# Kernel tuning notes

Hardware: AMD Instinct MI355X
Metric: run time of the kernel (lower is better)

## Reference

```python
import jax, jax.numpy as jnp
import numpy as np

N_HEAD = 16
D_MODEL = 1024
D_K = 64
D_V = 64
B = 8
L = 1024
EPS = 1e-5
NEG_INF = -1e9


def setup_inputs() -> dict:
    key = jax.random.key(0)
    ks = jax.random.split(key, 6)
    qkv_out = N_HEAD * (2 * D_K + D_V)  # 3072
    x = jax.random.normal(ks[0], (B, L, D_MODEL), dtype=jnp.float32)
    # causal attention mask (N, 1, L, L), 1 = keep, 0 = masked
    mask = jnp.broadcast_to(jnp.tril(jnp.ones((L, L), jnp.float32))[None, None], (B, 1, L, L))
    W_qkv = jax.random.normal(ks[1], (D_MODEL, qkv_out), dtype=jnp.float32) * 0.02
    b_qkv = jnp.zeros((qkv_out,), jnp.float32)
    W_proj = jax.random.normal(ks[2], (N_HEAD * D_V, D_MODEL), dtype=jnp.float32) * 0.02
    b_proj = jnp.zeros((D_MODEL,), jnp.float32)
    gamma = jnp.ones((D_MODEL,), jnp.float32)
    beta = jnp.zeros((D_MODEL,), jnp.float32)
    return {"x": x, "mask": mask, "W_qkv": W_qkv, "b_qkv": b_qkv,
            "W_proj": W_proj, "b_proj": b_proj, "gamma": gamma, "beta": beta}


def _layer_norm(x, gamma, beta):
    u = jnp.mean(x, axis=-1, keepdims=True)
    s = jnp.mean(jnp.square(x - u), axis=-1, keepdims=True)
    return gamma * (x - u) / jnp.sqrt(s + EPS) + beta


def reference(x, mask, W_qkv, b_qkv, W_proj, b_proj, gamma, beta):
    residual = x
    qkv = jnp.einsum('bld,df->blf', x, W_qkv) + b_qkv  # 1x1 Conv1D == pointwise linear
    q_l = N_HEAD * D_K
    q = qkv[:, :, :q_l]
    k = qkv[:, :, q_l:2 * q_l]
    v = qkv[:, :, 2 * q_l:]
    # split heads: (B, L, H*D) -> (B, H, L, D)
    q = q.reshape(B, L, N_HEAD, D_K).transpose(0, 2, 1, 3)
    k = k.reshape(B, L, N_HEAD, D_K).transpose(0, 2, 1, 3)
    v = v.reshape(B, L, N_HEAD, D_V).transpose(0, 2, 1, 3)
    temperature = np.power(D_K, 0.5)
    attn = jnp.einsum('bhqd,bhkd->bhqk', q, k) / temperature
    attn = mask * attn + (1.0 - mask) * NEG_INF
    attn = jax.nn.softmax(attn, axis=-1)  # dropout is identity in eval mode
    out = jnp.einsum('bhqk,bhkd->bhqd', attn, v)
    # merge heads: (B, H, L, Dv) -> (B, L, H*Dv)
    out = out.transpose(0, 2, 1, 3).reshape(B, L, N_HEAD * D_V)
    out = jnp.einsum('blf,fd->bld', out, W_proj) + b_proj
    out = _layer_norm(out + residual, gamma, beta)
    return out, attn
```

## Files before the change

### kernel.cpp

```cpp
#include <hip/hip_runtime.h>

typedef __attribute__((ext_vector_type(4))) float f32x4;
typedef __attribute__((ext_vector_type(8))) __bf16 bf16x8;
typedef __attribute__((ext_vector_type(8))) unsigned short ushort8;

static __device__ __forceinline__ unsigned short f2bf(float f) {
    unsigned int u = __float_as_uint(f);
    u += 0x7fffu + ((u >> 16) & 1u);
    return (unsigned short)(u >> 16);
}
static __device__ __forceinline__ float bf2f(unsigned short u) {
    return __uint_as_float((unsigned int)u << 16);
}
static __device__ __forceinline__ bf16x8 as_bf(ushort8 v) {
    union { ushort8 u; bf16x8 b; } x; x.u = v; return x.b;
}
static __device__ __forceinline__ void gll16(const void* g, void* l) {
    __builtin_amdgcn_global_load_lds(
        (const __attribute__((address_space(1))) void*)g,
        (__attribute__((address_space(3))) void*)l, 16, 0, 0);
}

__global__ void cvt_bf16(const float* __restrict__ in, unsigned short* __restrict__ out,
                         int n8) {
    int i = blockIdx.x * 256 + threadIdx.x;
    if (i >= n8) return;
    const float4* p = (const float4*)(in + (size_t)i * 8);
    float4 a = p[0], b = p[1];
    ushort8 o = { f2bf(a.x), f2bf(a.y), f2bf(a.z), f2bf(a.w),
                  f2bf(b.x), f2bf(b.y), f2bf(b.z), f2bf(b.w) };
    *(ushort8*)(out + (size_t)i * 8) = o;
}

__global__ void tconv_bf16(const float* __restrict__ in, unsigned short* __restrict__ out,
                           int K, int N) {
    __shared__ float t[64][65];
    const int tid = threadIdx.x;
    const int n0 = blockIdx.x * 64, k0 = blockIdx.y * 64;
#pragma unroll
    for (int i = 0; i < 4; i++) {
        int idx = tid + 256 * i;
        int r = idx >> 4, c4 = (idx & 15) * 4;
        float4 v = *(const float4*)(in + (size_t)(k0 + r) * N + n0 + c4);
        t[r][c4] = v.x; t[r][c4 + 1] = v.y; t[r][c4 + 2] = v.z; t[r][c4 + 3] = v.w;
    }
    __syncthreads();
#pragma unroll
    for (int i = 0; i < 2; i++) {
        int idx = tid + 256 * i;
        int nl = idx >> 3, k8 = (idx & 7) * 8;
        ushort8 o;
#pragma unroll
        for (int j = 0; j < 8; j++) o[j] = f2bf(t[k8 + j][nl]);
        *(ushort8*)(out + (size_t)(n0 + nl) * K + k0 + k8) = o;
    }
}

template <int EPI>
__global__ __launch_bounds__(256, 2)
void gemm_bf16(const unsigned short* __restrict__ A,
               const unsigned short* __restrict__ BT,
               const float* __restrict__ bias,
               unsigned short* __restrict__ qh, unsigned short* __restrict__ kh,
               unsigned short* __restrict__ vt,
               float* __restrict__ Cf,
               int K, int mtiles, int Ncols)
{
    __shared__ unsigned short smem[2 * 128 * 64];
    unsigned short* As = smem;
    unsigned short* Bs = smem + 128 * 64;

    const int tid = threadIdx.x;
    const int wid = tid >> 6, lane = tid & 63;
    const int g = lane >> 4, c = lane & 15;
    const int wr = (wid >> 1) * 64, wc = (wid & 1) * 64;

    const int nwg = gridDim.x;
    const int swz = ((int)blockIdx.x & 7) * (nwg >> 3) + ((int)blockIdx.x >> 3);
    const int bm = (swz % mtiles) * 128;
    const int bn = (swz / mtiles) * 128;

    const int srow = lane >> 3;
    const int scol8 = ((lane & 7) ^ srow) * 8;
    const size_t arow0 = (size_t)(bm + wid * 8 + srow);
    const size_t brow0 = (size_t)(bn + wid * 8 + srow);

    f32x4 acc[4][4] = {};

    for (int k0 = 0; k0 < K; k0 += 64) {
        __syncthreads();
#pragma unroll
        for (int t = 0; t < 4; t++) {
            gll16(A + (arow0 + t * 32) * K + k0 + scol8,
                  (char*)As + t * 4096 + wid * 1024);
            gll16(BT + (brow0 + t * 32) * K + k0 + scol8,
                  (char*)Bs + t * 4096 + wid * 1024);
        }
        __syncthreads();
#pragma unroll
        for (int ks = 0; ks < 2; ks++) {
            bf16x8 af[4], bfr[4];
#pragma unroll
            for (int mi = 0; mi < 4; mi++) {
                int row = wr + mi * 16 + c;
                int off = row * 128 + ((ks * 64 + g * 16) ^ ((c & 7) << 4));
                af[mi] = as_bf(*(const ushort8*)((const char*)As + off));
            }
#pragma unroll
            for (int ni = 0; ni < 4; ni++) {
                int row = wc + ni * 16 + c;
                int off = row * 128 + ((ks * 64 + g * 16) ^ ((c & 7) << 4));
                bfr[ni] = as_bf(*(const ushort8*)((const char*)Bs + off));
            }
#pragma unroll
            for (int mi = 0; mi < 4; mi++)
#pragma unroll
                for (int ni = 0; ni < 4; ni++)
                    acc[mi][ni] = __builtin_amdgcn_mfma_f32_16x16x32_bf16(
                        af[mi], bfr[ni], acc[mi][ni], 0, 0, 0);
        }
    }

    if (EPI == 1) {
#pragma unroll
        for (int mi = 0; mi < 4; mi++)
#pragma unroll
            for (int ni = 0; ni < 4; ni++)
#pragma unroll
                for (int r = 0; r < 4; r++) {
                    int m = bm + wr + mi * 16 + g * 4 + r;
                    int n = bn + wc + ni * 16 + c;
                    Cf[(size_t)m * Ncols + n] = acc[mi][ni][r] + bias[n];
                }
    } else {
        const int b = bm >> 10, lb = bm & 1023;
#pragma unroll
        for (int nh = 0; nh < 2; nh++) {
            int n0 = bn + nh * 64;
            int region = n0 >> 10;
            int h = (n0 & 1023) >> 6;
            __syncthreads();
            if (region < 2) {
                float qscale = (region == 0) ? 0.1803368801f : 1.0f;
                if ((wid & 1) == nh) {
#pragma unroll
                    for (int mi = 0; mi < 4; mi++)
#pragma unroll
                        for (int ni = 0; ni < 4; ni++)
#pragma unroll
                            for (int r = 0; r < 4; r++) {
                                int row = wr + mi * 16 + g * 4 + r;
                                int col = ni * 16 + c;
                                float v = (acc[mi][ni][r] + bias[n0 + col]) * qscale;
                                smem[row * 64 + col] = f2bf(v);
                            }
                }
                __syncthreads();
                unsigned short* dst = region == 0 ? qh : kh;
#pragma unroll
                for (int i = 0; i < 4; i++) {
                    int idx = tid + 256 * i;
                    int row = idx >> 3, c8 = (idx & 7) * 8;
                    ushort8 v = *(const ushort8*)&smem[row * 64 + c8];
                    *(ushort8*)(dst + ((size_t)((b * 16 + h) * 1024 + lb + row)) * 64 + c8) = v;
                }
            } else {
                if ((wid & 1) == nh) {
#pragma unroll
                    for (int mi = 0; mi < 4; mi++)
#pragma unroll
                        for (int ni = 0; ni < 4; ni++)
#pragma unroll
                            for (int r = 0; r < 4; r++) {
                                int l = wr + mi * 16 + g * 4 + r;
                                int d = ni * 16 + c;
                                float v = acc[mi][ni][r] + bias[n0 + d];
                                smem[d * 128 + (l ^ ((d & 7) << 3))] = f2bf(v);
                            }
                }
                __syncthreads();
#pragma unroll
                for (int i = 0; i < 4; i++) {
                    int idx = tid + 256 * i;
                    int d = idx >> 4, l8 = idx & 15;
                    ushort8 v = *(const ushort8*)&smem[d * 128 + ((l8 * 8) ^ ((d & 7) << 3))];
                    *(ushort8*)(vt + ((size_t)((b * 16 + h) * 64 + d)) * 1024 + lb + l8 * 8) = v;
                }
            }
        }
    }
}

__global__ __launch_bounds__(256, 3)
void attn_kernel(const unsigned short* __restrict__ qh,
                 const unsigned short* __restrict__ kh,
                 const unsigned short* __restrict__ vt,
                 float* __restrict__ attn, unsigned short* __restrict__ ob)
{
    __shared__ char smem[49152];

    const int bh = blockIdx.x;
    const int qt = blockIdx.y;
    const int q0 = qt * 64;
    const int ntiles = qt + 1;

    const int tid = threadIdx.x, wid = tid >> 6, lane = tid & 63;
    const int g = lane >> 4, c = lane & 15;

    const size_t baseKV = (size_t)bh * 65536;
    const int qrow = q0 + wid * 16 + c;

    bf16x8 qa[2];
    qa[0] = as_bf(*(const ushort8*)(qh + baseKV + (size_t)qrow * 64 + g * 8));
    qa[1] = as_bf(*(const ushort8*)(qh + baseKV + (size_t)qrow * 64 + 32 + g * 8));

    const int srow = lane >> 3;
    const int scol8 = ((lane & 7) ^ srow) * 8;

    float lsum = 0.f;
    {
        int cur = 0;
        const unsigned short* kb0 = kh + baseKV;
        gll16(kb0 + (size_t)(wid * 8 + srow) * 64 + scol8, smem + wid * 1024);
        gll16(kb0 + (size_t)(32 + wid * 8 + srow) * 64 + scol8, smem + 4096 + wid * 1024);
        __syncthreads();
        for (int kt = 0; kt < ntiles; ++kt) {
            if (kt + 1 < ntiles) {
                const unsigned short* kb = kh + baseKV + (size_t)(kt + 1) * 4096;
                char* dst = smem + (cur ^ 1) * 8192;
                gll16(kb + (size_t)(wid * 8 + srow) * 64 + scol8, dst + wid * 1024);
                gll16(kb + (size_t)(32 + wid * 8 + srow) * 64 + scol8, dst + 4096 + wid * 1024);
            }
            const char* Kc = smem + cur * 8192;
            __builtin_amdgcn_s_setprio(1);
#pragma unroll
            for (int a = 0; a < 4; a++) {
                int krow = a * 16 + c;
                f32x4 sa = {0.f, 0.f, 0.f, 0.f};
#pragma unroll
                for (int ks = 0; ks < 2; ks++) {
                    int off = krow * 128 + ((ks * 64 + g * 16) ^ ((c & 7) << 4));
                    bf16x8 kf = as_bf(*(const ushort8*)(Kc + off));
                    sa = __builtin_amdgcn_mfma_f32_16x16x32_bf16(kf, qa[ks], sa, 0, 0, 0);
                }
                int kb4 = kt * 64 + a * 16 + g * 4;
#pragma unroll
                for (int r = 0; r < 4; r++)
                    lsum += (kb4 + r > qrow) ? 0.f : __builtin_amdgcn_exp2f(sa[r]);
            }
            __builtin_amdgcn_s_setprio(0);
            __syncthreads();
            cur ^= 1;
        }
    }
    lsum += __shfl_xor(lsum, 16);
    lsum += __shfl_xor(lsum, 32);
    const float lr = -__log2f(lsum);

    float* attnB = attn + (size_t)bh * (1024 * 1024) + (size_t)q0 * 1024;
    f32x4 oacc[4] = {};
    {
        int cur = 0;
        const unsigned short* kb0 = kh + baseKV;
        const unsigned short* vb0 = vt + baseKV;
        gll16(kb0 + (size_t)(wid * 8 + srow) * 64 + scol8, smem + wid * 1024);
        gll16(kb0 + (size_t)(32 + wid * 8 + srow) * 64 + scol8, smem + 4096 + wid * 1024);
        gll16(vb0 + (size_t)(wid * 8 + srow) * 1024 + scol8, smem + 16384 + wid * 1024);
        gll16(vb0 + (size_t)(32 + wid * 8 + srow) * 1024 + scol8, smem + 20480 + wid * 1024);
        __syncthreads();

        for (int kt = 0; kt < ntiles; ++kt) {
            if (kt + 1 < ntiles) {
                const unsigned short* kb = kh + baseKV + (size_t)(kt + 1) * 4096;
                const unsigned short* vb = vt + baseKV + (kt + 1) * 64;
                char* kdst = smem + (cur ^ 1) * 8192;
                char* vdst = smem + 16384 + (cur ^ 1) * 8192;
                gll16(kb + (size_t)(wid * 8 + srow) * 64 + scol8, kdst + wid * 1024);
                gll16(kb + (size_t)(32 + wid * 8 + srow) * 64 + scol8, kdst + 4096 + wid * 1024);
                gll16(vb + (size_t)(wid * 8 + srow) * 1024 + scol8, vdst + wid * 1024);
                gll16(vb + (size_t)(32 + wid * 8 + srow) * 1024 + scol8, vdst + 4096 + wid * 1024);
            }
            const char* Kc = smem + cur * 8192;
            const char* Vc = smem + 16384 + cur * 8192;
            char* Pc = smem + 32768 + cur * 8192;
            char* Pw = Pc + wid * 2048;

#pragma unroll
            for (int a = 0; a < 4; a++) {
                int krow = a * 16 + c;
                f32x4 sa = {0.f, 0.f, 0.f, 0.f};
#pragma unroll
                for (int ks = 0; ks < 2; ks++) {
                    int off = krow * 128 + ((ks * 64 + g * 16) ^ ((c & 7) << 4));
                    bf16x8 kf = as_bf(*(const ushort8*)(Kc + off));
                    sa = __builtin_amdgcn_mfma_f32_16x16x32_bf16(kf, qa[ks], sa, 0, 0, 0);
                }
                int kb4 = kt * 64 + a * 16 + g * 4;
                float p0 = __builtin_amdgcn_exp2f((kb4 + 0 > qrow) ? -1e9f : sa[0] + lr);
                float p1 = __builtin_amdgcn_exp2f((kb4 + 1 > qrow) ? -1e9f : sa[1] + lr);
                float p2 = __builtin_amdgcn_exp2f((kb4 + 2 > qrow) ? -1e9f : sa[2] + lr);
                float p3 = __builtin_amdgcn_exp2f((kb4 + 3 > qrow) ? -1e9f : sa[3] + lr);
                uint2 pw;
                asm("v_cvt_pk_bf16_f32 %0, %1, %2" : "=v"(pw.x) : "v"(p0), "v"(p1));
                asm("v_cvt_pk_bf16_f32 %0, %1, %2" : "=v"(pw.y) : "v"(p2), "v"(p3));
                *(uint2*)(Pw + c * 128 + ((a * 32 + g * 8) ^ ((c & 7) << 4))) = pw;
            }

            __builtin_amdgcn_s_setprio(1);
#pragma unroll
            for (int ks = 0; ks < 2; ks++) {
                int aoff = c * 128 + ((ks * 64 + g * 16) ^ ((c & 7) << 4));
                bf16x8 pa = as_bf(*(const ushort8*)(Pw + aoff));
#pragma unroll
                for (int ni = 0; ni < 4; ni++) {
                    int d = ni * 16 + c;
                    int voff = d * 128 + ((ks * 64 + g * 16) ^ ((d & 7) << 4));
                    bf16x8 vf = as_bf(*(const ushort8*)(Vc + voff));
                    oacc[ni] = __builtin_amdgcn_mfma_f32_16x16x32_bf16(pa, vf, oacc[ni], 0, 0, 0);
                }
            }
            __builtin_amdgcn_s_setprio(0);
            __syncthreads();

#pragma unroll
            for (int i = 0; i < 2; i++) {
                int idx = tid + 256 * i;
                int row = idx >> 3, c16 = idx & 7;
                int off = (row >> 4) * 2048 + (row & 15) * 128 + ((c16 * 16) ^ ((row & 7) << 4));
                ushort8 v = *(const ushort8*)(Pc + off);
                float4 f0 = { bf2f(v[0]), bf2f(v[1]), bf2f(v[2]), bf2f(v[3]) };
                float4 f1 = { bf2f(v[4]), bf2f(v[5]), bf2f(v[6]), bf2f(v[7]) };
                float* dp = attnB + (size_t)row * 1024 + kt * 64 + c16 * 8;
                *(float4*)dp = f0;
                *(float4*)(dp + 4) = f1;
            }
            cur ^= 1;
        }
    }

    {
        float4 z = {0.f, 0.f, 0.f, 0.f};
        for (int kt = ntiles; kt < 16; ++kt) {
#pragma unroll
            for (int i = 0; i < 4; i++) {
                int idx = tid + 256 * i;
                int row = idx >> 4, c4 = (idx & 15) << 2;
                *(float4*)(attnB + (size_t)row * 1024 + kt * 64 + c4) = z;
            }
        }
    }

    __syncthreads();
#pragma unroll
    for (int ni = 0; ni < 4; ni++)
#pragma unroll
        for (int r = 0; r < 4; r++) {
            int row = wid * 16 + g * 4 + r;
            int d = ni * 16 + c;
            int off = row * 128 + ((d * 2) ^ ((row & 7) << 4));
            *(unsigned short*)(smem + off) = f2bf(oacc[ni][r]);
        }
    __syncthreads();
    {
        const int b = bh >> 4, h = bh & 15;
#pragma unroll
        for (int i = 0; i < 2; i++) {
            int idx = tid + 256 * i;
            int row = idx >> 3, c8 = idx & 7;
            int off = row * 128 + ((c8 * 16) ^ ((row & 7) << 4));
            ushort8 v = *(const ushort8*)(smem + off);
            *(ushort8*)(ob + ((size_t)(b * 1024 + q0 + row)) * 1024 + h * 64 + c8 * 8) = v;
        }
    }
}

__global__ __launch_bounds__(256, 2)
void ln_kernel(const float* __restrict__ y, const float* __restrict__ x,
               const float* __restrict__ gamma, const float* __restrict__ beta,
               float* __restrict__ out)
{
    const int m = blockIdx.x;
    const int tid = threadIdx.x;
    const int wid = tid >> 6, lane = tid & 63;
    float4 vy = *(const float4*)(y + (size_t)m * 1024 + tid * 4);
    float4 vx = *(const float4*)(x + (size_t)m * 1024 + tid * 4);
    float4 v = {vy.x + vx.x, vy.y + vx.y, vy.z + vx.z, vy.w + vx.w};
    float s1 = v.x + v.y + v.z + v.w;
    float s2 = v.x * v.x + v.y * v.y + v.z * v.z + v.w * v.w;
#pragma unroll
    for (int d = 1; d < 64; d <<= 1) {
        s1 += __shfl_xor(s1, d);
        s2 += __shfl_xor(s2, d);
    }
    __shared__ float red1[4], red2[4];
    if (lane == 0) { red1[wid] = s1; red2[wid] = s2; }
    __syncthreads();
    float t1 = red1[0] + red1[1] + red1[2] + red1[3];
    float t2 = red2[0] + red2[1] + red2[2] + red2[3];
    float mean = t1 * (1.f / 1024.f);
    float var = t2 * (1.f / 1024.f) - mean * mean;
    float rstd = rsqrtf(var + 1e-5f);
    float4 g4 = *(const float4*)(gamma + tid * 4);
    float4 b4 = *(const float4*)(beta + tid * 4);
    float4 o;
    o.x = g4.x * (v.x - mean) * rstd + b4.x;
    o.y = g4.y * (v.y - mean) * rstd + b4.y;
    o.z = g4.z * (v.z - mean) * rstd + b4.z;
    o.w = g4.w * (v.w - mean) * rstd + b4.w;
    *(float4*)(out + (size_t)m * 1024 + tid * 4) = o;
}

extern "C" void kernel_launch(void* const* d_in, const int* in_sizes, int n_in,
                              void* d_out, int out_size, void* d_ws, size_t ws_size,
                              hipStream_t stream)
{
    const float* x      = (const float*)d_in[0];
    const float* W_qkv  = (const float*)d_in[2];
    const float* b_qkv  = (const float*)d_in[3];
    const float* W_proj = (const float*)d_in[4];
    const float* b_proj = (const float*)d_in[5];
    const float* gamma  = (const float*)d_in[6];
    const float* beta   = (const float*)d_in[7];

    float* out  = (float*)d_out;
    float* attn = out + (size_t)8 * 1024 * 1024;

    const size_t E = (size_t)8192 * 1024;
    unsigned short* ws = (unsigned short*)d_ws;
    unsigned short* qh     = ws;
    unsigned short* kh     = qh + E;
    unsigned short* vt     = kh + E;
    unsigned short* xb     = vt + E;
    unsigned short* wqkvT  = xb + E;
    unsigned short* wprojT = wqkvT + (size_t)3072 * 1024;
    unsigned short* ob     = wprojT + (size_t)1024 * 1024;
    float* yb   = (float*)(void*)qh;

    cvt_bf16<<<4096, 256, 0, stream>>>(x, xb, (int)(E / 8));
    tconv_bf16<<<dim3(48, 16), 256, 0, stream>>>(W_qkv, wqkvT, 1024, 3072);
    tconv_bf16<<<dim3(16, 16), 256, 0, stream>>>(W_proj, wprojT, 1024, 1024);

    gemm_bf16<0><<<1536, 256, 0, stream>>>(xb, wqkvT, b_qkv,
                                           qh, kh, vt, nullptr, 1024, 64, 3072);
    attn_kernel<<<dim3(128, 16), 256, 0, stream>>>(qh, kh, vt, attn, ob);
    gemm_bf16<1><<<512, 256, 0, stream>>>(ob, wprojT, b_proj,
                                          nullptr, nullptr, nullptr, yb, 1024, 64, 1024);
    ln_kernel<<<8192, 256, 0, stream>>>(yb, x, gamma, beta, out);
}
```

Before: 273.1 us.

## Use 256x256-tile, 8-wave double-buffered GEMM for QKV projection

Replaces the 128x128-tile QKV GEMM with a dedicated 256x256-tile kernel using 512 threads, BK=32 double-buffered global_load_lds staging, an XOR-swizzled LDS layout and raised wave priority around the MFMA block. Each wave now writes its head-split Q/K/V^T epilogue through a private LDS slice, so the per-half block-wide barriers go away. Larger tiles raise arithmetic intensity and cut global traffic per FLOP. In exchange the grid has only 384 blocks, which may give uneven wave occupancy across CUs, and register pressure is higher with 32 accumulators per wave.

```diff
diff --git a/kernel.cpp b/kernel.cpp
--- a/kernel.cpp
+++ b/kernel.cpp
@@ -56,15 +56,167 @@
     }
 }
 
-template <int EPI>
+__global__ __launch_bounds__(512, 2)
+void gemm256_qkv(const unsigned short* __restrict__ A,
+                 const unsigned short* __restrict__ BT,
+                 const float* __restrict__ bias,
+                 unsigned short* __restrict__ qh, unsigned short* __restrict__ kh,
+                 unsigned short* __restrict__ vt, int K)
+{
+    __shared__ char smem[65536];
+    const int tid = threadIdx.x;
+    const int wid = tid >> 6, lane = tid & 63;
+    const int g = lane >> 4, c = lane & 15;
+    const int wr = (wid >> 2) * 128;
+    const int wc = (wid & 3) * 64;
+
+    const int nwg = gridDim.x;
+    const int swz = ((int)blockIdx.x & 7) * (nwg >> 3) + ((int)blockIdx.x >> 3);
+    const int bm = (swz & 31) * 256;
+    const int bn = (swz >> 5) * 256;
+
+    const int sch   = (lane & 7) ^ (lane >> 3);
+    const int srow2 = ((lane >> 3) << 1) + (sch >> 2);
+    const int scol  = (sch & 3) * 8;
+    const int fbase = (c >> 1) * 128 + (((((c & 1) << 2) | g) ^ (c >> 1)) * 16);
+
+    f32x4 acc[8][4] = {};
+
+    auto stage = [&](int p, int kt) {
+        const int k0 = kt * 32;
+        char* bufA = smem + p * 32768;
+        char* bufB = bufA + 16384;
+#pragma unroll
+        for (int half = 0; half < 2; half++) {
+            const int PRb = half * 64;
+            const int rbase = PRb * 2 + wid * 16 + srow2;
+            gll16(A + (size_t)(bm + rbase) * K + k0 + scol,
+                  bufA + (PRb + wid * 8) * 128);
+            gll16(BT + (size_t)(bn + rbase) * K + k0 + scol,
+                  bufB + (PRb + wid * 8) * 128);
+        }
+    };
+
+    const int NT = K >> 5;
+    stage(0, 0);
+    stage(1, 1);
+
+    for (int kt = 0; kt < NT - 1; ++kt) {
+        asm volatile("s_waitcnt vmcnt(4)" ::: "memory");
+        __builtin_amdgcn_s_barrier();
+        const char* bufA = smem + (kt & 1) * 32768;
+        const char* bufB = bufA + 16384;
+        bf16x8 af[8], bf[4];
+#pragma unroll
+        for (int mi = 0; mi < 8; mi++)
+            af[mi] = as_bf(*(const ushort8*)(bufA + wr * 64 + mi * 1024 + fbase));
+#pragma unroll
+        for (int ni = 0; ni < 4; ni++)
+            bf[ni] = as_bf(*(const ushort8*)(bufB + wc * 64 + ni * 1024 + fbase));
+        asm volatile("s_waitcnt lgkmcnt(0)" ::: "memory");
+        __builtin_amdgcn_sched_barrier(0);
+        __builtin_amdgcn_s_barrier();
+        if (kt + 2 < NT) stage(kt & 1, kt + 2);
+        __builtin_amdgcn_sched_barrier(0);
+        __builtin_amdgcn_s_setprio(1);
+#pragma unroll
+        for (int mi = 0; mi < 8; mi++)
+#pragma unroll
+            for (int ni = 0; ni < 4; ni++)
+                acc[mi][ni] = __builtin_amdgcn_mfma_f32_16x16x32_bf16(
+                    af[mi], bf[ni], acc[mi][ni], 0, 0, 0);
+        __builtin_amdgcn_s_setprio(0);
+    }
+    {
+        asm volatile("s_waitcnt vmcnt(0)" ::: "memory");
+        __builtin_amdgcn_s_barrier();
+        const char* bufA = smem + ((NT - 1) & 1) * 32768;
+        const char* bufB = bufA + 16384;
+        bf16x8 af[8], bf[4];
+#pragma unroll
+        for (int mi = 0; mi < 8; mi++)
+            af[mi] = as_bf(*(const ushort8*)(bufA + wr * 64 + mi * 1024 + fbase));
+#pragma unroll
+        for (int ni = 0; ni < 4; ni++)
+            bf[ni] = as_bf(*(const ushort8*)(bufB + wc * 64 + ni * 1024 + fbase));
+        asm volatile("s_waitcnt lgkmcnt(0)" ::: "memory");
+        __builtin_amdgcn_sched_barrier(0);
+        __builtin_amdgcn_s_barrier();
+#pragma unroll
+        for (int mi = 0; mi < 8; mi++)
+#pragma unroll
+            for (int ni = 0; ni < 4; ni++)
+                acc[mi][ni] = __builtin_amdgcn_mfma_f32_16x16x32_bf16(
+                    af[mi], bf[ni], acc[mi][ni], 0, 0, 0);
+    }
+
+    const int n0 = bn + wc;
+    const int region = n0 >> 10;
+    const int h = (n0 & 1023) >> 6;
+    const int b = bm >> 10;
+    const int lb = bm & 1023;
+    const float qscale = (region == 0) ? 0.1803368801f : 1.0f;
+    char* W = smem + wid * 8192;
+
+    if (region < 2) {
+        unsigned short* dst = (region == 0) ? qh : kh;
+#pragma unroll
+        for (int hh = 0; hh < 2; hh++) {
+#pragma unroll
+            for (int mi2 = 0; mi2 < 4; mi2++) {
+                int mi = hh * 4 + mi2;
+#pragma unroll
+                for (int ni = 0; ni < 4; ni++)
+#pragma unroll
+                    for (int r = 0; r < 4; r++) {
+                        int row = mi2 * 16 + g * 4 + r;
+                        int col = ni * 16 + c;
+                        float v = (acc[mi][ni][r] + bias[n0 + col]) * qscale;
+                        *(unsigned short*)(W + row * 128 + ((col * 2) ^ ((row & 7) << 4))) = f2bf(v);
+                    }
+            }
+#pragma unroll
+            for (int j = 0; j < 8; j++) {
+                int cid = j * 64 + lane;
+                int row = cid >> 3, c8 = cid & 7;
+                ushort8 v = *(const ushort8*)(W + row * 128 + ((c8 * 16) ^ ((row & 7) << 4)));
+                int l = lb + wr + hh * 64 + row;
+                *(ushort8*)(dst + ((size_t)((b * 16 + h) * 1024 + l)) * 64 + c8 * 8) = v;
+            }
+        }
+    } else {
+#pragma unroll
+        for (int hh = 0; hh < 2; hh++) {
+#pragma unroll
+            for (int mi2 = 0; mi2 < 4; mi2++) {
+                int mi = hh * 4 + mi2;
+#pragma unroll
+                for (int ni = 0; ni < 4; ni++)
+#pragma unroll
+                    for (int r = 0; r < 4; r++) {
+                        int ll = mi2 * 16 + g * 4 + r;
+                        int d = ni * 16 + c;
+                        float v = acc[mi][ni][r] + bias[n0 + d];
+                        *(unsigned short*)(W + d * 128 + ((ll * 2) ^ ((d & 7) << 4))) = f2bf(v);
+                    }
+            }
+#pragma unroll
+            for (int j = 0; j < 8; j++) {
+                int cid = j * 64 + lane;
+                int drow = cid >> 3, c8 = cid & 7;
+                ushort8 v = *(const ushort8*)(W + drow * 128 + ((c8 * 16) ^ ((drow & 7) << 4)));
+                *(ushort8*)(vt + ((size_t)((b * 16 + h) * 64 + drow)) * 1024
+                            + (lb + wr + hh * 64) + c8 * 8) = v;
+            }
+        }
+    }
+}
+
 __global__ __launch_bounds__(256, 2)
-void gemm_bf16(const unsigned short* __restrict__ A,
-               const unsigned short* __restrict__ BT,
-               const float* __restrict__ bias,
-               unsigned short* __restrict__ qh, unsigned short* __restrict__ kh,
-               unsigned short* __restrict__ vt,
-               float* __restrict__ Cf,
-               int K, int mtiles, int Ncols)
+void gemm128_f32(const unsigned short* __restrict__ A,
+                 const unsigned short* __restrict__ BT,
+                 const float* __restrict__ bias,
+                 float* __restrict__ Cf, int K, int mtiles, int Ncols)
 {
     __shared__ unsigned short smem[2 * 128 * 64];
     unsigned short* As = smem;
@@ -121,74 +273,16 @@
         }
     }
 
-    if (EPI == 1) {
-#pragma unroll
-        for (int mi = 0; mi < 4; mi++)
-#pragma unroll
-            for (int ni = 0; ni < 4; ni++)
-#pragma unroll
-                for (int r = 0; r < 4; r++) {
-                    int m = bm + wr + mi * 16 + g * 4 + r;
-                    int n = bn + wc + ni * 16 + c;
-                    Cf[(size_t)m * Ncols + n] = acc[mi][ni][r] + bias[n];
-                }
-    } else {
-        const int b = bm >> 10, lb = bm & 1023;
-#pragma unroll
-        for (int nh = 0; nh < 2; nh++) {
-            int n0 = bn + nh * 64;
-            int region = n0 >> 10;
-            int h = (n0 & 1023) >> 6;
-            __syncthreads();
-            if (region < 2) {
-                float qscale = (region == 0) ? 0.1803368801f : 1.0f;
-                if ((wid & 1) == nh) {
-#pragma unroll
-                    for (int mi = 0; mi < 4; mi++)
-#pragma unroll
-                        for (int ni = 0; ni < 4; ni++)
-#pragma unroll
-                            for (int r = 0; r < 4; r++) {
-                                int row = wr + mi * 16 + g * 4 + r;
-                                int col = ni * 16 + c;
-                                float v = (acc[mi][ni][r] + bias[n0 + col]) * qscale;
-                                smem[row * 64 + col] = f2bf(v);
-                            }
-                }
-                __syncthreads();
-                unsigned short* dst = region == 0 ? qh : kh;
-#pragma unroll
-                for (int i = 0; i < 4; i++) {
-                    int idx = tid + 256 * i;
-                    int row = idx >> 3, c8 = (idx & 7) * 8;
-                    ushort8 v = *(const ushort8*)&smem[row * 64 + c8];
-                    *(ushort8*)(dst + ((size_t)((b * 16 + h) * 1024 + lb + row)) * 64 + c8) = v;
-                }
-            } else {
-                if ((wid & 1) == nh) {
-#pragma unroll
-                    for (int mi = 0; mi < 4; mi++)
-#pragma unroll
-                        for (int ni = 0; ni < 4; ni++)
-#pragma unroll
-                            for (int r = 0; r < 4; r++) {
-                                int l = wr + mi * 16 + g * 4 + r;
-                                int d = ni * 16 + c;
-                                float v = acc[mi][ni][r] + bias[n0 + d];
-                                smem[d * 128 + (l ^ ((d & 7) << 3))] = f2bf(v);
-                            }
-                }
-                __syncthreads();
-#pragma unroll
-                for (int i = 0; i < 4; i++) {
-                    int idx = tid + 256 * i;
-                    int d = idx >> 4, l8 = idx & 15;
-                    ushort8 v = *(const ushort8*)&smem[d * 128 + ((l8 * 8) ^ ((d & 7) << 3))];
-                    *(ushort8*)(vt + ((size_t)((b * 16 + h) * 64 + d)) * 1024 + lb + l8 * 8) = v;
-                }
-            }
-        }
-    }
+#pragma unroll
+    for (int mi = 0; mi < 4; mi++)
+#pragma unroll
+        for (int ni = 0; ni < 4; ni++)
+#pragma unroll
+            for (int r = 0; r < 4; r++) {
+                int m = bm + wr + mi * 16 + g * 4 + r;
+                int n = bn + wc + ni * 16 + c;
+                Cf[(size_t)m * Ncols + n] = acc[mi][ni][r] + bias[n];
+            }
 }
 
 __global__ __launch_bounds__(256, 3)
@@ -440,10 +534,8 @@
     tconv_bf16<<<dim3(48, 16), 256, 0, stream>>>(W_qkv, wqkvT, 1024, 3072);
     tconv_bf16<<<dim3(16, 16), 256, 0, stream>>>(W_proj, wprojT, 1024, 1024);
 
-    gemm_bf16<0><<<1536, 256, 0, stream>>>(xb, wqkvT, b_qkv,
-                                           qh, kh, vt, nullptr, 1024, 64, 3072);
+    gemm256_qkv<<<384, 512, 0, stream>>>(xb, wqkvT, b_qkv, qh, kh, vt, 1024);
     attn_kernel<<<dim3(128, 16), 256, 0, stream>>>(qh, kh, vt, attn, ob);
-    gemm_bf16<1><<<512, 256, 0, stream>>>(ob, wprojT, b_proj,
-                                          nullptr, nullptr, nullptr, yb, 1024, 64, 1024);
+    gemm128_f32<<<512, 256, 0, stream>>>(ob, wprojT, b_proj, yb, 1024, 64, 1024);
     ln_kernel<<<8192, 256, 0, stream>>>(yb, x, gamma, beta, out);
 }
```

Result: no change. 271.1 us (-0.7%).
